# Optimization experiments

Measured on AMD Instinct MI355X. Metric: run time of the kernel, lower is better.

## Reference

```python
import jax, jax.numpy as jnp
import numpy as np

NUM_HEAD = 8

def conv1x1(x, W, b):
    # x: (n, c, h, w); W: (o, c); b: (o,)
    return jnp.einsum('nchw,oc->nohw', x, W) + b[None, :, None, None]

def setup_inputs() -> dict:
    key = jax.random.key(0)
    ks = jax.random.split(key, 9)
    n, C, H, Wd = 16, 512, 64, 64
    KC, VC = 256, 512
    s = lambda fan_in: 1.0 / np.sqrt(fan_in)
    return {
        'x':  jax.random.normal(ks[0], (n, C, H, Wd), dtype=jnp.float32),
        'Wk': jax.random.normal(ks[1], (KC, C), dtype=jnp.float32) * s(C),
        'bk': jnp.zeros((KC,), dtype=jnp.float32),
        'Wq': jax.random.normal(ks[2], (KC, C), dtype=jnp.float32) * s(C),
        'bq': jnp.zeros((KC,), dtype=jnp.float32),
        'Wv': jax.random.normal(ks[3], (VC, C), dtype=jnp.float32) * s(C),
        'bv': jnp.zeros((VC,), dtype=jnp.float32),
        'We': jax.random.normal(ks[4], (C, VC), dtype=jnp.float32) * s(VC),
        'be': jnp.zeros((C,), dtype=jnp.float32),
    }

def reference(x, Wk, bk, Wq, bq, Wv, bv, We, be):
    n, c, h, w = x.shape
    L = h * w
    Hn = NUM_HEAD
    key   = conv1x1(x, Wk, bk).reshape(n, Hn, -1, L)   # (n, H, hk, L)
    query = conv1x1(x, Wq, bq).reshape(n, Hn, -1, L)   # (n, H, hk, L)
    value = conv1x1(x, Wv, bv).reshape(n, Hn, -1, L)   # (n, H, hv, L)
    key_sm   = jax.nn.softmax(key, axis=3)              # softmax over spatial
    query_sm = jax.nn.softmax(query, axis=2)            # softmax over head channels
    # linear attention: (value @ key^T) @ query, no LxL matrix
    context = jnp.einsum('nhvl,nhkl->nhvk', value, key_sm)     # (n, H, hv, hk)
    att = jnp.einsum('nhvk,nhkl->nhvl', context, query_sm)     # (n, H, hv, L)
    att = att.reshape(n, -1, h, w)                              # (n, VC, h, w)
    return x + conv1x1(att, We, be)
```

## Files before the change

kernel.cpp:

```cpp
#include <hip/hip_runtime.h>
#include <cstddef>
#include <cstdint>

#define N_BATCH 16
#define C_IN    512
#define L       4096
#define KC      256
#define VC      512
#define NH      8
#define HK      32
#define HV      64
#define CTX_CHUNKS 8
#define CHUNK_L (L / CTX_CHUNKS)

using f32x4 = __attribute__((ext_vector_type(4))) float;
using s16x8 = __attribute__((ext_vector_type(8))) short;

static __device__ inline ushort f2bf(float f) {
  uint32_t u = __float_as_uint(f);
  uint32_t r = (u + 0x7FFFu + ((u >> 16) & 1u)) >> 16;
  return (ushort)r;
}
static __device__ inline float bf2f(ushort u) {
  return __uint_as_float((uint32_t)u << 16);
}

__global__ __launch_bounds__(256) void k_prep_w(
    const float* __restrict__ Wk, const float* __restrict__ bk,
    const float* __restrict__ Wq, const float* __restrict__ bq,
    const float* __restrict__ Wv, const float* __restrict__ bv,
    ushort* __restrict__ Wb, float* __restrict__ bb)
{
  const int o = blockIdx.x;
  const float* src; const float* bsrc; int oo;
  if (o < 256)      { src = Wk + (size_t)o * C_IN;         bsrc = bk; oo = o; }
  else if (o < 512) { src = Wq + (size_t)(o - 256) * C_IN; bsrc = bq; oo = o - 256; }
  else              { src = Wv + (size_t)(o - 512) * C_IN; bsrc = bv; oo = o - 512; }
  const int t = threadIdx.x;
  Wb[(size_t)o * C_IN + t * 2]     = f2bf(src[t * 2]);
  Wb[(size_t)o * C_IN + t * 2 + 1] = f2bf(src[t * 2 + 1]);
  if (t == 0) bb[o] = bsrc[oo];
}

__global__ __launch_bounds__(256) void k_prep_x(const float* __restrict__ x,
                                                ushort* __restrict__ xT)
{
  __shared__ float t[64][65];
  const int n = blockIdx.z, cy = blockIdx.y, lx = blockIdx.x;
  const float* xp = x + ((size_t)n * C_IN + cy * 64) * L + (size_t)lx * 64;
  const int l4 = (threadIdx.x & 15) * 4;
  const int c0 = threadIdx.x >> 4;
  #pragma unroll
  for (int i = 0; i < 4; ++i) {
    int cc = c0 + i * 16;
    f32x4 v = *(const f32x4*)&xp[(size_t)cc * L + l4];
    t[cc][l4]     = v[0];
    t[cc][l4 + 1] = v[1];
    t[cc][l4 + 2] = v[2];
    t[cc][l4 + 3] = v[3];
  }
  __syncthreads();
  ushort* op = xT + ((size_t)n * L + lx * 64) * C_IN + cy * 64;
  const int cp = (threadIdx.x & 15) * 4;
  const int l0 = threadIdx.x >> 4;
  #pragma unroll
  for (int i = 0; i < 4; ++i) {
    int lr = l0 + i * 16;
    uint2 pk;
    pk.x = (uint32_t)f2bf(t[cp][lr])     | ((uint32_t)f2bf(t[cp + 1][lr]) << 16);
    pk.y = (uint32_t)f2bf(t[cp + 2][lr]) | ((uint32_t)f2bf(t[cp + 3][lr]) << 16);
    *(uint2*)(op + (size_t)lr * C_IN + cp) = pk;
  }
}

#define QBM 256
#define QBN 256
#define QBK 64

__global__ __launch_bounds__(512) void k_qkv_mfma(
    const ushort* __restrict__ Wb,
    const ushort* __restrict__ xT,
    const float* __restrict__ bb,
    ushort* __restrict__ kqv,
    ushort* __restrict__ qT)
{
  extern __shared__ __align__(16) char smem[];
  const int n  = blockIdx.z;
  const int oy = blockIdx.y;
  const int lx = blockIdx.x;
  const int tid  = threadIdx.x;
  const int wave = tid >> 6, lane = tid & 63;
  const int wr = wave >> 2, wc = wave & 3;

  f32x4 acc[8][4] = {};

  const ushort* gA = Wb + (size_t)(oy * QBM) * C_IN;
  const ushort* gB = xT + ((size_t)n * L + lx * QBN) * C_IN;

  const int srow = lane >> 3;
  const int sslotbase = lane & 7;

  #define QSTAGE(buf, k0)                                                        \
    {                                                                            \
      ushort* As_ = (ushort*)(smem + (buf) * 65536);                             \
      ushort* Bs_ = (ushort*)(smem + (buf) * 65536 + 32768);                     \
      _Pragma("unroll")                                                          \
      for (int i_ = 0; i_ < 4; ++i_) {                                           \
        int rbase_ = wave * 32 + i_ * 8;                                         \
        int row_ = rbase_ + srow;                                                \
        int ss_ = sslotbase ^ (row_ & 7);                                        \
        __builtin_amdgcn_global_load_lds(                                        \
            (const __attribute__((address_space(1))) uint32_t*)(gA + (size_t)row_ * C_IN + (k0) + ss_ * 8), \
            (__attribute__((address_space(3))) uint32_t*)(As_ + rbase_ * QBK),   \
            16, 0, 0);                                                           \
        __builtin_amdgcn_global_load_lds(                                        \
            (const __attribute__((address_space(1))) uint32_t*)(gB + (size_t)row_ * C_IN + (k0) + ss_ * 8), \
            (__attribute__((address_space(3))) uint32_t*)(Bs_ + rbase_ * QBK),   \
            16, 0, 0);                                                           \
      }                                                                          \
    }

  QSTAGE(0, 0)

  const int nt = C_IN / QBK;
  for (int t = 0; t < nt; ++t) {
    if (t < nt - 1) {
      QSTAGE((t + 1) & 1, (t + 1) * QBK)
      asm volatile("s_waitcnt vmcnt(8)" ::: "memory");
    } else {
      asm volatile("s_waitcnt vmcnt(0)" ::: "memory");
    }
    __builtin_amdgcn_s_barrier();
    asm volatile("" ::: "memory");
    ushort* As = (ushort*)(smem + (t & 1) * 65536);
    ushort* Bs = (ushort*)(smem + (t & 1) * 65536 + 32768);
    __builtin_amdgcn_s_setprio(1);
    #pragma unroll
    for (int ks = 0; ks < 2; ++ks) {
      s16x8 af[8], bfr[4];
      #pragma unroll
      for (int m = 0; m < 8; ++m) {
        int row = wr * 128 + m * 16 + (lane & 15);
        int slot = (ks * 4 + (lane >> 4)) ^ (row & 7);
        af[m] = *(const s16x8*)&As[row * QBK + slot * 8];
      }
      #pragma unroll
      for (int nn = 0; nn < 4; ++nn) {
        int row = wc * 64 + nn * 16 + (lane & 15);
        int slot = (ks * 4 + (lane >> 4)) ^ (row & 7);
        bfr[nn] = *(const s16x8*)&Bs[row * QBK + slot * 8];
      }
      #pragma unroll
      for (int m = 0; m < 8; ++m)
        #pragma unroll
        for (int nn = 0; nn < 4; ++nn)
          acc[m][nn] = __builtin_amdgcn_mfma_f32_16x16x32_bf16(af[m], bfr[nn], acc[m][nn], 0, 0, 0);
    }
    __builtin_amdgcn_s_setprio(0);
    asm volatile("" ::: "memory");
    __builtin_amdgcn_s_barrier();
  }
  #undef QSTAGE

  if (oy != 1) {
    float* ep = (float*)smem + wave * (16 * 68);
    const int erow = lane >> 4;
    const int ecol = lane & 15;
    const float* bias = bb + oy * QBM + wr * 128;
    ushort* outp = kqv + ((size_t)n * 1024 + oy * QBM + wr * 128) * L
                 + (size_t)lx * QBN + wc * 64;
    #pragma unroll
    for (int m = 0; m < 8; ++m) {
      #pragma unroll
      for (int nn = 0; nn < 4; ++nn)
        #pragma unroll
        for (int r = 0; r < 4; ++r)
          ep[(erow * 4 + r) * 68 + nn * 16 + ecol] = acc[m][nn][r];
      #pragma unroll
      for (int p = 0; p < 4; ++p) {
        int row = p * 4 + erow;
        f32x4 v = *(const f32x4*)&ep[row * 68 + ecol * 4];
        float bo = bias[m * 16 + row];
        uint2 pk;
        pk.x = (uint32_t)f2bf(v[0] + bo) | ((uint32_t)f2bf(v[1] + bo) << 16);
        pk.y = (uint32_t)f2bf(v[2] + bo) | ((uint32_t)f2bf(v[3] + bo) << 16);
        *(uint2*)&outp[(size_t)(m * 16 + row) * L + ecol * 4] = pk;
      }
    }
  } else {
    const float* bias = bb + 256 + wr * 128;
    ushort* qbase = qT + (size_t)n * L * KC;
    const int g4 = (lane >> 4) * 4;
    #pragma unroll
    for (int hp = 0; hp < 4; ++hp) {
      const int m0 = 2 * hp, m1 = 2 * hp + 1;
      const float b0_0 = bias[m0 * 16 + g4 + 0], b0_1 = bias[m0 * 16 + g4 + 1];
      const float b0_2 = bias[m0 * 16 + g4 + 2], b0_3 = bias[m0 * 16 + g4 + 3];
      const float b1_0 = bias[m1 * 16 + g4 + 0], b1_1 = bias[m1 * 16 + g4 + 1];
      const float b1_2 = bias[m1 * 16 + g4 + 2], b1_3 = bias[m1 * 16 + g4 + 3];
      #pragma unroll
      for (int nn = 0; nn < 4; ++nn) {
        float v0[4], v1[4];
        v0[0] = acc[m0][nn][0] + b0_0; v0[1] = acc[m0][nn][1] + b0_1;
        v0[2] = acc[m0][nn][2] + b0_2; v0[3] = acc[m0][nn][3] + b0_3;
        v1[0] = acc[m1][nn][0] + b1_0; v1[1] = acc[m1][nn][1] + b1_1;
        v1[2] = acc[m1][nn][2] + b1_2; v1[3] = acc[m1][nn][3] + b1_3;
        float mx = fmaxf(fmaxf(fmaxf(v0[0], v0[1]), fmaxf(v0[2], v0[3])),
                         fmaxf(fmaxf(v1[0], v1[1]), fmaxf(v1[2], v1[3])));
        mx = fmaxf(mx, __shfl_xor(mx, 16));
        mx = fmaxf(mx, __shfl_xor(mx, 32));
        float e0[4], e1[4];
        float s = 0.f;
        #pragma unroll
        for (int r = 0; r < 4; ++r) { e0[r] = __expf(v0[r] - mx); s += e0[r]; }
        #pragma unroll
        for (int r = 0; r < 4; ++r) { e1[r] = __expf(v1[r] - mx); s += e1[r]; }
        s += __shfl_xor(s, 16);
        s += __shfl_xor(s, 32);
        float inv = 1.0f / s;
        int l = lx * QBN + wc * 64 + nn * 16 + (lane & 15);
        ushort* dst = qbase + (size_t)l * KC + wr * 128;
        uint2 p0, p1;
        p0.x = (uint32_t)f2bf(e0[0] * inv) | ((uint32_t)f2bf(e0[1] * inv) << 16);
        p0.y = (uint32_t)f2bf(e0[2] * inv) | ((uint32_t)f2bf(e0[3] * inv) << 16);
        p1.x = (uint32_t)f2bf(e1[0] * inv) | ((uint32_t)f2bf(e1[1] * inv) << 16);
        p1.y = (uint32_t)f2bf(e1[2] * inv) | ((uint32_t)f2bf(e1[3] * inv) << 16);
        *(uint2*)&dst[m0 * 16 + g4] = p0;
        *(uint2*)&dst[m1 * 16 + g4] = p1;
      }
    }
  }
}

__device__ inline float blockReduceMax(float v, float* red) {
  #pragma unroll
  for (int off = 32; off > 0; off >>= 1)
    v = fmaxf(v, __shfl_down(v, off, 64));
  int tid = threadIdx.x;
  if ((tid & 63) == 0) red[tid >> 6] = v;
  __syncthreads();
  return fmaxf(fmaxf(red[0], red[1]), fmaxf(red[2], red[3]));
}
__device__ inline float blockReduceSum(float v, float* red) {
  #pragma unroll
  for (int off = 32; off > 0; off >>= 1)
    v += __shfl_down(v, off, 64);
  int tid = threadIdx.x;
  if ((tid & 63) == 0) red[tid >> 6] = v;
  __syncthreads();
  return red[0] + red[1] + red[2] + red[3];
}

__global__ __launch_bounds__(256) void k_kstats(const ushort* __restrict__ kqv,
                                                float* __restrict__ kmax,
                                                float* __restrict__ kinv)
{
  const int r = blockIdx.x;
  const int n = blockIdx.y;
  const ushort* row = kqv + ((size_t)n * 1024 + r) * L;
  __shared__ float red1[4];
  __shared__ float red2[4];
  const int tid = threadIdx.x;
  s16x8 a = *(const s16x8*)(row + tid * 16);
  s16x8 b = *(const s16x8*)(row + tid * 16 + 8);
  float v[16];
  #pragma unroll
  for (int j = 0; j < 8; ++j) { v[j] = bf2f((ushort)a[j]); v[8 + j] = bf2f((ushort)b[j]); }
  float m = -3.0e38f;
  #pragma unroll
  for (int j = 0; j < 16; ++j) m = fmaxf(m, v[j]);
  m = blockReduceMax(m, red1);
  float s = 0.f;
  #pragma unroll
  for (int j = 0; j < 16; ++j) s += __expf(v[j] - m);
  s = blockReduceSum(s, red2);
  if (tid == 0) { kmax[n * KC + r] = m; kinv[n * KC + r] = 1.0f / s; }
}

__global__ __launch_bounds__(256) void k_ctx_mfma(const ushort* __restrict__ kqv,
                                                  const float* __restrict__ kmax,
                                                  const float* __restrict__ kinv,
                                                  float* __restrict__ ctxpart)
{
  const int chunk = blockIdx.x;
  const int nh    = blockIdx.y;
  const int n = nh >> 3, h = nh & 7;
  const int tid = threadIdx.x, wave = tid >> 6, lane = tid & 63;

  __shared__ __align__(16) ushort Ks[32 * 64];
  __shared__ __align__(16) ushort Vs[64 * 64];
  __shared__ float km[32], kv[32];

  if (tid < 32) { km[tid] = kmax[nh * 32 + tid]; kv[tid] = kinv[nh * 32 + tid]; }
  __syncthreads();

  const ushort* Kp = kqv + ((size_t)n * 1024 + h * HK) * L + (size_t)chunk * CHUNK_L;
  const ushort* Vp = kqv + ((size_t)n * 1024 + 512 + h * HV) * L + (size_t)chunk * CHUNK_L;

  const int krow = tid >> 3;
  const int kslot = (tid & 7) ^ (krow & 7);
  f32x4 acc[2] = {};

  for (int step = 0; step < 8; ++step) {
    const int l0 = step * 64;
    #pragma unroll
    for (int j = 0; j < 2; ++j) {
      int vr = (j * 4 + wave) * 8 + (lane >> 3);
      int vslot = (lane & 7) ^ (vr & 7);
      __builtin_amdgcn_global_load_lds(
          (const __attribute__((address_space(1))) uint32_t*)(Vp + (size_t)vr * L + l0 + vslot * 8),
          (__attribute__((address_space(3))) uint32_t*)(Vs + (size_t)(j * 4 + wave) * 512),
          16, 0, 0);
    }
    s16x8 kvec = *(const s16x8*)(Kp + (size_t)krow * L + l0 + (tid & 7) * 8);
    float mk = km[krow], ik = kv[krow];
    s16x8 w;
    #pragma unroll
    for (int j = 0; j < 8; ++j) {
      float f = bf2f((ushort)kvec[j]);
      w[j] = (short)f2bf(__expf(f - mk) * ik);
    }
    *(s16x8*)&Ks[krow * 64 + kslot * 8] = w;
    __syncthreads();

    #pragma unroll
    for (int ks = 0; ks < 2; ++ks) {
      int arow = wave * 16 + (lane & 15);
      int aslot = (ks * 4 + (lane >> 4)) ^ (arow & 7);
      s16x8 af = *(const s16x8*)&Vs[arow * 64 + aslot * 8];
      #pragma unroll
      for (int nf = 0; nf < 2; ++nf) {
        int brow = nf * 16 + (lane & 15);
        int bslot = (ks * 4 + (lane >> 4)) ^ (brow & 7);
        s16x8 bfr = *(const s16x8*)&Ks[brow * 64 + bslot * 8];
        acc[nf] = __builtin_amdgcn_mfma_f32_16x16x32_bf16(af, bfr, acc[nf], 0, 0, 0);
      }
    }
    __syncthreads();
  }

  float* outp = ctxpart + ((size_t)nh * CTX_CHUNKS + chunk) * (HV * HK);
  #pragma unroll
  for (int nf = 0; nf < 2; ++nf) {
    #pragma unroll
    for (int r = 0; r < 4; ++r) {
      int v = wave * 16 + (lane >> 4) * 4 + r;
      int k = nf * 16 + (lane & 15);
      outp[v * HK + k] = acc[nf][r];
    }
  }
}

__global__ __launch_bounds__(256) void k_m(const float* __restrict__ ctxpart,
                                           const float* __restrict__ We,
                                           ushort* __restrict__ Mbuf)
{
  const int h = blockIdx.x;
  const int n = blockIdx.y;
  const int nh = n * 8 + h;
  const int tid = threadIdx.x;
  __shared__ float ctx[64][32];

  #pragma unroll
  for (int i = 0; i < 8; ++i) {
    int e = tid + i * 256;
    float s = 0.f;
    for (int c = 0; c < CTX_CHUNKS; ++c)
      s += ctxpart[((size_t)nh * CTX_CHUNKS + c) * (HV * HK) + e];
    ((float*)ctx)[e] = s;
  }
  __syncthreads();

  const int k  = tid & 31;
  const int og = tid >> 5;
  for (int j = 0; j < 64; ++j) {
    int o = og * 64 + j;
    const float* we = We + (size_t)o * VC + h * HV;
    float s = 0.f;
    #pragma unroll
    for (int v = 0; v < 64; ++v) s += we[v] * ctx[v][k];
    Mbuf[((size_t)n * 512 + o) * KC + h * HK + k] = f2bf(s);
  }
}

#define BM 128
#define BN 128
#define BK 32

__global__ __launch_bounds__(256) void k_final_mfma(
    const ushort* __restrict__ Mb,
    const ushort* __restrict__ qT,
    const float* __restrict__ x,
    const float* __restrict__ be,
    float* __restrict__ out)
{
  const int n  = blockIdx.z;
  const int oy = blockIdx.y;
  const int lx = blockIdx.x;
  const int tid  = threadIdx.x;
  const int wave = tid >> 6, lane = tid & 63;
  const int wr = wave >> 1, wc = wave & 1;

  __shared__ __align__(16) char smem[32768 + 17408];

  f32x4 acc[4][4] = {};

  const ushort* gA = Mb + ((size_t)n * 512 + oy * BM) * KC;
  const ushort* gB = qT + ((size_t)n * L + lx * BN) * KC;

  const int r0 = wave * 32;
  const int lrow = lane >> 2;

  #define FSTAGE(buf, k0)                                                        \
    {                                                                            \
      ushort* As_ = (ushort*)(smem + (buf) * 16384);                             \
      ushort* Bs_ = (ushort*)(smem + (buf) * 16384 + 8192);                      \
      _Pragma("unroll")                                                          \
      for (int i_ = 0; i_ < 2; ++i_) {                                           \
        int row_ = r0 + i_ * 16 + lrow;                                          \
        int ss_ = (lane & 3) ^ ((row_ >> 1) & 3);                                \
        __builtin_amdgcn_global_load_lds(                                        \
            (const __attribute__((address_space(1))) uint32_t*)(gA + (size_t)row_ * KC + (k0) + ss_ * 8), \
            (__attribute__((address_space(3))) uint32_t*)(As_ + (r0 + i_ * 16) * BK), \
            16, 0, 0);                                                           \
        __builtin_amdgcn_global_load_lds(                                        \
            (const __attribute__((address_space(1))) uint32_t*)(gB + (size_t)row_ * KC + (k0) + ss_ * 8), \
            (__attribute__((address_space(3))) uint32_t*)(Bs_ + (r0 + i_ * 16) * BK), \
            16, 0, 0);                                                           \
      }                                                                          \
    }

  FSTAGE(0, 0)

  const int nt = KC / BK;
  for (int t = 0; t < nt; ++t) {
    if (t < nt - 1) {
      FSTAGE((t + 1) & 1, (t + 1) * BK)
      asm volatile("s_waitcnt vmcnt(4)" ::: "memory");
    } else {
      asm volatile("s_waitcnt vmcnt(0)" ::: "memory");
    }
    __builtin_amdgcn_s_barrier();
    asm volatile("" ::: "memory");
    ushort* As = (ushort*)(smem + (t & 1) * 16384);
    ushort* Bs = (ushort*)(smem + (t & 1) * 16384 + 8192);
    s16x8 af[4], bfr[4];
    #pragma unroll
    for (int m = 0; m < 4; ++m) {
      int row = wr * 64 + m * 16 + (lane & 15);
      int slot = (lane >> 4) ^ ((row >> 1) & 3);
      af[m] = *(const s16x8*)&As[row * BK + slot * 8];
    }
    #pragma unroll
    for (int nn = 0; nn < 4; ++nn) {
      int row = wc * 64 + nn * 16 + (lane & 15);
      int slot = (lane >> 4) ^ ((row >> 1) & 3);
      bfr[nn] = *(const s16x8*)&Bs[row * BK + slot * 8];
    }
    __builtin_amdgcn_s_setprio(1);
    #pragma unroll
    for (int m = 0; m < 4; ++m)
      #pragma unroll
      for (int nn = 0; nn < 4; ++nn)
        acc[m][nn] = __builtin_amdgcn_mfma_f32_16x16x32_bf16(af[m], bfr[nn], acc[m][nn], 0, 0, 0);
    __builtin_amdgcn_s_setprio(0);
    asm volatile("" ::: "memory");
    __builtin_amdgcn_s_barrier();
  }
  #undef FSTAGE

  float* ep = (float*)(smem + 32768) + wave * (16 * 68);
  const int erow = lane >> 4;
  const int ecol = lane & 15;
  const float* bias = be + oy * BM + wr * 64;
  const float* xp = x + ((size_t)n * 512 + oy * BM + wr * 64) * L
                  + (size_t)lx * BN + wc * 64;
  float* op = out + ((size_t)n * 512 + oy * BM + wr * 64) * L
            + (size_t)lx * BN + wc * 64;
  #pragma unroll
  for (int m = 0; m < 4; ++m) {
    #pragma unroll
    for (int nn = 0; nn < 4; ++nn)
      #pragma unroll
      for (int r = 0; r < 4; ++r)
        ep[(erow * 4 + r) * 68 + nn * 16 + ecol] = acc[m][nn][r];
    #pragma unroll
    for (int p = 0; p < 4; ++p) {
      int row = p * 4 + erow;
      f32x4 v = *(const f32x4*)&ep[row * 68 + ecol * 4];
      float bo = bias[m * 16 + row];
      f32x4 xv = *(const f32x4*)&xp[(size_t)(m * 16 + row) * L + ecol * 4];
      v = v + xv + bo;
      *(f32x4*)&op[(size_t)(m * 16 + row) * L + ecol * 4] = v;
    }
  }
}

extern "C" void kernel_launch(void* const* d_in, const int* in_sizes, int n_in,
                              void* d_out, int out_size, void* d_ws, size_t ws_size,
                              hipStream_t stream)
{
  const float* x  = (const float*)d_in[0];
  const float* Wk = (const float*)d_in[1];
  const float* bk = (const float*)d_in[2];
  const float* Wq = (const float*)d_in[3];
  const float* bq = (const float*)d_in[4];
  const float* Wv = (const float*)d_in[5];
  const float* bv = (const float*)d_in[6];
  const float* We = (const float*)d_in[7];
  const float* be = (const float*)d_in[8];
  float* out = (float*)d_out;

  char* ws = (char*)d_ws;
  size_t off = 0;
  ushort* kqv  = (ushort*)(ws + off); off += (size_t)N_BATCH * 1024 * L * 2;
  ushort* xT   = (ushort*)(ws + off); off += (size_t)N_BATCH * L * C_IN * 2;
  ushort* Wb   = (ushort*)(ws + off); off += (size_t)1024 * C_IN * 2;
  float*  bb   = (float*)(ws + off);  off += (size_t)1024 * 4;
  float*  kmax = (float*)(ws + off);  off += (size_t)N_BATCH * KC * 4;
  float*  kinv = (float*)(ws + off);  off += (size_t)N_BATCH * KC * 4;
  ushort* qT   = (ushort*)(ws + off); off += (size_t)N_BATCH * L * KC * 2;
  float*  ctxp = (float*)(ws + off);  off += (size_t)N_BATCH * NH * CTX_CHUNKS * HV * HK * 4;
  ushort* Mbuf = (ushort*)(ws + off); off += (size_t)N_BATCH * 512 * KC * 2;

  (void)hipFuncSetAttribute((const void*)k_qkv_mfma,
                            hipFuncAttributeMaxDynamicSharedMemorySize, 131072);

  k_prep_w<<<dim3(1024), 256, 0, stream>>>(Wk, bk, Wq, bq, Wv, bv, Wb, bb);
  k_prep_x<<<dim3(64, 8, N_BATCH), 256, 0, stream>>>(x, xT);
  k_qkv_mfma<<<dim3(16, 4, N_BATCH), 512, 131072, stream>>>(Wb, xT, bb, kqv, qT);
  k_kstats<<<dim3(KC, N_BATCH), 256, 0, stream>>>(kqv, kmax, kinv);
  k_ctx_mfma<<<dim3(CTX_CHUNKS, N_BATCH * NH), 256, 0, stream>>>(kqv, kmax, kinv, ctxp);
  k_m<<<dim3(NH, N_BATCH), 256, 0, stream>>>(ctxp, We, Mbuf);
  k_final_mfma<<<dim3(32, 4, N_BATCH), 256, 0, stream>>>(Mbuf, qT, x, be, out);
}
```

Baseline: 267.0 us.

## Split GEMM main loop into quadrant phases interleaving half-tile loads with MFMA

Restructures the projection GEMM main loop so each K step is split into four MFMA quadrants, with the next tile's A/B halves staged between them and finer-grained vmcnt waits and barriers. This spreads global-to-LDS traffic across compute and lowers the fragment register footprint. The wave-to-tile mapping changes to interleaved 16-row/16-col strips, which requires the query softmax epilogue to combine partial max/sum across two waves through shared memory. This adds more barriers and an extra LDS reduction step.

```diff
diff --git a/kernel.cpp b/kernel.cpp
--- a/kernel.cpp
+++ b/kernel.cpp
@@ -97,136 +97,176 @@
   const ushort* gA = Wb + (size_t)(oy * QBM) * C_IN;
   const ushort* gB = xT + ((size_t)n * L + lx * QBN) * C_IN;
 
-  const int srow = lane >> 3;
-  const int sslotbase = lane & 7;
-
-  #define QSTAGE(buf, k0)                                                        \
+  const int srow8 = lane >> 3;
+  const int lane7 = lane & 7;
+
+  #define STAGE_HALF(buf, k0, isA, rh)                                           \
     {                                                                            \
-      ushort* As_ = (ushort*)(smem + (buf) * 65536);                             \
-      ushort* Bs_ = (ushort*)(smem + (buf) * 65536 + 32768);                     \
+      ushort* S_ = (ushort*)(smem + (buf) * 65536 + ((isA) ? 0 : 32768));        \
+      const ushort* G_ = (isA) ? gA : gB;                                        \
       _Pragma("unroll")                                                          \
-      for (int i_ = 0; i_ < 4; ++i_) {                                           \
-        int rbase_ = wave * 32 + i_ * 8;                                         \
-        int row_ = rbase_ + srow;                                                \
-        int ss_ = sslotbase ^ (row_ & 7);                                        \
+      for (int i_ = 0; i_ < 2; ++i_) {                                           \
+        int rb_ = (rh) + wave * 16 + i_ * 8;                                     \
+        int row_ = rb_ + srow8;                                                  \
+        int ss_ = lane7 ^ (row_ & 7);                                            \
         __builtin_amdgcn_global_load_lds(                                        \
-            (const __attribute__((address_space(1))) uint32_t*)(gA + (size_t)row_ * C_IN + (k0) + ss_ * 8), \
-            (__attribute__((address_space(3))) uint32_t*)(As_ + rbase_ * QBK),   \
-            16, 0, 0);                                                           \
-        __builtin_amdgcn_global_load_lds(                                        \
-            (const __attribute__((address_space(1))) uint32_t*)(gB + (size_t)row_ * C_IN + (k0) + ss_ * 8), \
-            (__attribute__((address_space(3))) uint32_t*)(Bs_ + rbase_ * QBK),   \
+            (const __attribute__((address_space(1))) uint32_t*)(G_ + (size_t)row_ * C_IN + (k0) + ss_ * 8), \
+            (__attribute__((address_space(3))) uint32_t*)(S_ + rb_ * QBK),       \
             16, 0, 0);                                                           \
       }                                                                          \
     }
 
-  QSTAGE(0, 0)
+  #define WAITV(nn) asm volatile("s_waitcnt vmcnt(" #nn ")" ::: "memory")
+  #define BARX() do { asm volatile("" ::: "memory");                             \
+                      __builtin_amdgcn_s_barrier();                              \
+                      asm volatile("" ::: "memory"); } while (0)
+
+  s16x8 afr[4][2], bf01[2][2], bf23[2][2];
+
+  #define READ_A(As_, fbase)                                                     \
+    _Pragma("unroll")                                                            \
+    for (int q_ = 0; q_ < 4; ++q_)                                               \
+      _Pragma("unroll")                                                          \
+      for (int ks_ = 0; ks_ < 2; ++ks_) {                                        \
+        int row_ = ((fbase) + q_) * 32 + wr * 16 + (lane & 15);                  \
+        int slot_ = (ks_ * 4 + (lane >> 4)) ^ (row_ & 7);                        \
+        afr[q_][ks_] = *(const s16x8*)&(As_)[row_ * QBK + slot_ * 8];            \
+      }
+  #define READ_B(Bs_, dst, gbase)                                                \
+    _Pragma("unroll")                                                            \
+    for (int j_ = 0; j_ < 2; ++j_)                                               \
+      _Pragma("unroll")                                                          \
+      for (int ks_ = 0; ks_ < 2; ++ks_) {                                        \
+        int row_ = ((gbase) + j_) * 64 + wc * 16 + (lane & 15);                  \
+        int slot_ = (ks_ * 4 + (lane >> 4)) ^ (row_ & 7);                        \
+        dst[j_][ks_] = *(const s16x8*)&(Bs_)[row_ * QBK + slot_ * 8];            \
+      }
+  #define MFMA_Q(fbase, gbase, bfrag)                                            \
+    __builtin_amdgcn_s_setprio(1);                                               \
+    _Pragma("unroll")                                                            \
+    for (int q_ = 0; q_ < 4; ++q_)                                               \
+      _Pragma("unroll")                                                          \
+      for (int j_ = 0; j_ < 2; ++j_)                                             \
+        _Pragma("unroll")                                                        \
+        for (int ks_ = 0; ks_ < 2; ++ks_)                                        \
+          acc[(fbase) + q_][(gbase) + j_] = __builtin_amdgcn_mfma_f32_16x16x32_bf16( \
+              afr[q_][ks_], bfrag[j_][ks_], acc[(fbase) + q_][(gbase) + j_], 0, 0, 0); \
+    __builtin_amdgcn_s_setprio(0);
+
+  STAGE_HALF(0, 0, 1, 0)
+  STAGE_HALF(0, 0, 0, 0)
+  STAGE_HALF(0, 0, 0, 128)
+  STAGE_HALF(0, 0, 1, 128)
 
   const int nt = C_IN / QBK;
   for (int t = 0; t < nt; ++t) {
-    if (t < nt - 1) {
-      QSTAGE((t + 1) & 1, (t + 1) * QBK)
-      asm volatile("s_waitcnt vmcnt(8)" ::: "memory");
-    } else {
-      asm volatile("s_waitcnt vmcnt(0)" ::: "memory");
-    }
-    __builtin_amdgcn_s_barrier();
-    asm volatile("" ::: "memory");
-    ushort* As = (ushort*)(smem + (t & 1) * 65536);
-    ushort* Bs = (ushort*)(smem + (t & 1) * 65536 + 32768);
-    __builtin_amdgcn_s_setprio(1);
-    #pragma unroll
-    for (int ks = 0; ks < 2; ++ks) {
-      s16x8 af[8], bfr[4];
-      #pragma unroll
-      for (int m = 0; m < 8; ++m) {
-        int row = wr * 128 + m * 16 + (lane & 15);
-        int slot = (ks * 4 + (lane >> 4)) ^ (row & 7);
-        af[m] = *(const s16x8*)&As[row * QBK + slot * 8];
-      }
-      #pragma unroll
-      for (int nn = 0; nn < 4; ++nn) {
-        int row = wc * 64 + nn * 16 + (lane & 15);
-        int slot = (ks * 4 + (lane >> 4)) ^ (row & 7);
-        bfr[nn] = *(const s16x8*)&Bs[row * QBK + slot * 8];
-      }
-      #pragma unroll
-      for (int m = 0; m < 8; ++m)
-        #pragma unroll
-        for (int nn = 0; nn < 4; ++nn)
-          acc[m][nn] = __builtin_amdgcn_mfma_f32_16x16x32_bf16(af[m], bfr[nn], acc[m][nn], 0, 0, 0);
-    }
-    __builtin_amdgcn_s_setprio(0);
-    asm volatile("" ::: "memory");
-    __builtin_amdgcn_s_barrier();
-  }
-  #undef QSTAGE
+    const int cb = t & 1, nb = cb ^ 1;
+    const int kn = (t + 1) * QBK;
+    ushort* As = (ushort*)(smem + cb * 65536);
+    ushort* Bs = (ushort*)(smem + cb * 65536 + 32768);
+    const bool st = t < nt - 1;
+    if (st) STAGE_HALF(nb, kn, 1, 0)
+    WAITV(4); BARX();
+    READ_A(As, 0) READ_B(Bs, bf01, 0)
+    MFMA_Q(0, 0, bf01)
+    BARX();
+    if (st) { STAGE_HALF(nb, kn, 0, 0) WAITV(4); } else { WAITV(2); }
+    BARX();
+    READ_B(Bs, bf23, 2)
+    MFMA_Q(0, 2, bf23)
+    BARX();
+    if (st) { STAGE_HALF(nb, kn, 0, 128) WAITV(4); } else { WAITV(0); }
+    BARX();
+    READ_A(As, 4)
+    MFMA_Q(4, 0, bf01)
+    BARX();
+    if (st) STAGE_HALF(nb, kn, 1, 128)
+    BARX();
+    MFMA_Q(4, 2, bf23)
+    BARX();
+  }
+  #undef STAGE_HALF
+  #undef READ_A
+  #undef READ_B
+  #undef MFMA_Q
 
   if (oy != 1) {
     float* ep = (float*)smem + wave * (16 * 68);
     const int erow = lane >> 4;
     const int ecol = lane & 15;
-    const float* bias = bb + oy * QBM + wr * 128;
-    ushort* outp = kqv + ((size_t)n * 1024 + oy * QBM + wr * 128) * L
-                 + (size_t)lx * QBN + wc * 64;
+    const float* bias = bb + oy * QBM;
+    ushort* outp = kqv + ((size_t)n * 1024 + oy * QBM) * L + (size_t)lx * QBN;
+    const int grun = ecol >> 2;
+    const int coff = (ecol & 3) * 4;
     #pragma unroll
     for (int m = 0; m < 8; ++m) {
       #pragma unroll
-      for (int nn = 0; nn < 4; ++nn)
+      for (int g = 0; g < 4; ++g)
         #pragma unroll
         for (int r = 0; r < 4; ++r)
-          ep[(erow * 4 + r) * 68 + nn * 16 + ecol] = acc[m][nn][r];
+          ep[(erow * 4 + r) * 68 + g * 16 + ecol] = acc[m][g][r];
       #pragma unroll
       for (int p = 0; p < 4; ++p) {
-        int row = p * 4 + erow;
-        f32x4 v = *(const f32x4*)&ep[row * 68 + ecol * 4];
-        float bo = bias[m * 16 + row];
+        int row16 = p * 4 + erow;
+        f32x4 v = *(const f32x4*)&ep[row16 * 68 + ecol * 4];
+        int orow = m * 32 + wr * 16 + row16;
+        int ocol = grun * 64 + wc * 16 + coff;
+        float bo = bias[orow];
         uint2 pk;
         pk.x = (uint32_t)f2bf(v[0] + bo) | ((uint32_t)f2bf(v[1] + bo) << 16);
         pk.y = (uint32_t)f2bf(v[2] + bo) | ((uint32_t)f2bf(v[3] + bo) << 16);
-        *(uint2*)&outp[(size_t)(m * 16 + row) * L + ecol * 4] = pk;
+        *(uint2*)&outp[(size_t)orow * L + ocol] = pk;
       }
     }
   } else {
-    const float* bias = bb + 256 + wr * 128;
+    const float* bias = bb + 256;
     ushort* qbase = qT + (size_t)n * L * KC;
     const int g4 = (lane >> 4) * 4;
-    #pragma unroll
-    for (int hp = 0; hp < 4; ++hp) {
-      const int m0 = 2 * hp, m1 = 2 * hp + 1;
-      const float b0_0 = bias[m0 * 16 + g4 + 0], b0_1 = bias[m0 * 16 + g4 + 1];
-      const float b0_2 = bias[m0 * 16 + g4 + 2], b0_3 = bias[m0 * 16 + g4 + 3];
-      const float b1_0 = bias[m1 * 16 + g4 + 0], b1_1 = bias[m1 * 16 + g4 + 1];
-      const float b1_2 = bias[m1 * 16 + g4 + 2], b1_3 = bias[m1 * 16 + g4 + 3];
-      #pragma unroll
-      for (int nn = 0; nn < 4; ++nn) {
-        float v0[4], v1[4];
-        v0[0] = acc[m0][nn][0] + b0_0; v0[1] = acc[m0][nn][1] + b0_1;
-        v0[2] = acc[m0][nn][2] + b0_2; v0[3] = acc[m0][nn][3] + b0_3;
-        v1[0] = acc[m1][nn][0] + b1_0; v1[1] = acc[m1][nn][1] + b1_1;
-        v1[2] = acc[m1][nn][2] + b1_2; v1[3] = acc[m1][nn][3] + b1_3;
-        float mx = fmaxf(fmaxf(fmaxf(v0[0], v0[1]), fmaxf(v0[2], v0[3])),
-                         fmaxf(fmaxf(v1[0], v1[1]), fmaxf(v1[2], v1[3])));
+    float* pmax = (float*)smem;
+    float* psum = (float*)smem + 4096;
+    __syncthreads();
+    #pragma unroll
+    for (int f = 0; f < 8; ++f) {
+      #pragma unroll
+      for (int j = 0; j < 4; ++j) {
+        float v[4];
+        #pragma unroll
+        for (int r = 0; r < 4; ++r)
+          v[r] = acc[f][j][r] + bias[f * 32 + wr * 16 + g4 + r];
+        float mx = fmaxf(fmaxf(v[0], v[1]), fmaxf(v[2], v[3]));
         mx = fmaxf(mx, __shfl_xor(mx, 16));
         mx = fmaxf(mx, __shfl_xor(mx, 32));
-        float e0[4], e1[4];
         float s = 0.f;
         #pragma unroll
-        for (int r = 0; r < 4; ++r) { e0[r] = __expf(v0[r] - mx); s += e0[r]; }
-        #pragma unroll
-        for (int r = 0; r < 4; ++r) { e1[r] = __expf(v1[r] - mx); s += e1[r]; }
+        for (int r = 0; r < 4; ++r) s += __expf(v[r] - mx);
         s += __shfl_xor(s, 16);
         s += __shfl_xor(s, 32);
-        float inv = 1.0f / s;
-        int l = lx * QBN + wc * 64 + nn * 16 + (lane & 15);
-        ushort* dst = qbase + (size_t)l * KC + wr * 128;
-        uint2 p0, p1;
-        p0.x = (uint32_t)f2bf(e0[0] * inv) | ((uint32_t)f2bf(e0[1] * inv) << 16);
-        p0.y = (uint32_t)f2bf(e0[2] * inv) | ((uint32_t)f2bf(e0[3] * inv) << 16);
-        p1.x = (uint32_t)f2bf(e1[0] * inv) | ((uint32_t)f2bf(e1[1] * inv) << 16);
-        p1.y = (uint32_t)f2bf(e1[2] * inv) | ((uint32_t)f2bf(e1[3] * inv) << 16);
-        *(uint2*)&dst[m0 * 16 + g4] = p0;
-        *(uint2*)&dst[m1 * 16 + g4] = p1;
+        int idx = (((f * 4 + j) * 4 + wc) * 16 + (lane & 15)) * 2 + wr;
+        pmax[idx] = mx;
+        psum[idx] = s;
+      }
+    }
+    __syncthreads();
+    #pragma unroll
+    for (int f = 0; f < 8; ++f) {
+      #pragma unroll
+      for (int j = 0; j < 4; ++j) {
+        int idx = (((f * 4 + j) * 4 + wc) * 16 + (lane & 15)) * 2 + wr;
+        float mw = pmax[idx],     sw = psum[idx];
+        float mo = pmax[idx ^ 1], so = psum[idx ^ 1];
+        float M = fmaxf(mw, mo);
+        float tot = sw * __expf(mw - M) + so * __expf(mo - M);
+        float inv = 1.0f / tot;
+        float e[4];
+        #pragma unroll
+        for (int r = 0; r < 4; ++r)
+          e[r] = __expf(acc[f][j][r] + bias[f * 32 + wr * 16 + g4 + r] - M) * inv;
+        int l = lx * QBN + j * 64 + wc * 16 + (lane & 15);
+        ushort* dst = qbase + (size_t)l * KC + f * 32 + wr * 16 + g4;
+        uint2 pk;
+        pk.x = (uint32_t)f2bf(e[0]) | ((uint32_t)f2bf(e[1]) << 16);
+        pk.y = (uint32_t)f2bf(e[2]) | ((uint32_t)f2bf(e[3]) << 16);
+        *(uint2*)dst = pk;
       }
     }
   }
```

Result: slower. 275.1 us (+3.0%).
